# Optimization experiments

Measured on AMD Instinct MI355X. Metric: run time of the kernel, lower is better.

The kernel has to match this reference:

```python
import jax, jax.numpy as jnp
import numpy as np

B, T, F = 64, 96, 32          # batch, window_size, num_features
H_ENC, H_DEC = 128, 128       # encoder / decoder hidden sizes


def _lstm_cell(x, h, c, k, r, b):
    # Keras LSTMCell math: gates ordered i, f, g(candidate), o
    z = x @ k + h @ r + b
    i, f, g, o = jnp.split(z, 4, axis=-1)
    i = jax.nn.sigmoid(i)
    f = jax.nn.sigmoid(f)
    g = jnp.tanh(g)
    o = jax.nn.sigmoid(o)
    c_new = f * c + i * g
    h_new = o * jnp.tanh(c_new)
    return h_new, c_new


def setup_inputs() -> dict:
    key = jax.random.key(0)
    ks = jax.random.split(key, 20)
    s = 0.05
    d = {
        "inputs": jax.random.normal(ks[0], (B, T, F), jnp.float32),
        # encoder LSTMCell (input dim = F)
        "enc_k": jax.random.normal(ks[1], (F, 4 * H_ENC), jnp.float32) * s,
        "enc_r": jax.random.normal(ks[2], (H_ENC, 4 * H_ENC), jnp.float32) * s,
        "enc_b": jnp.zeros((4 * H_ENC,), jnp.float32),
        # encoder attention MLP: in = 2*H_ENC + T -> H_ENC -> 1
        "ae_w1": jax.random.normal(ks[3], (2 * H_ENC + T, H_ENC), jnp.float32) * s,
        "ae_b1": jnp.zeros((H_ENC,), jnp.float32),
        "ae_w2": jax.random.normal(ks[4], (H_ENC, 1), jnp.float32) * s,
        "ae_b2": jnp.zeros((1,), jnp.float32),
        # decoder LSTMCell (input dim = H_DEC, the fc output)
        "dec_k": jax.random.normal(ks[5], (H_DEC, 4 * H_DEC), jnp.float32) * s,
        "dec_r": jax.random.normal(ks[6], (H_DEC, 4 * H_DEC), jnp.float32) * s,
        "dec_b": jnp.zeros((4 * H_DEC,), jnp.float32),
        # decoder attention MLP: in = 2*H_DEC + H_ENC -> H_ENC -> 1
        "ad_w1": jax.random.normal(ks[7], (2 * H_DEC + H_ENC, H_ENC), jnp.float32) * s,
        "ad_b1": jnp.zeros((H_ENC,), jnp.float32),
        "ad_w2": jax.random.normal(ks[8], (H_ENC, 1), jnp.float32) * s,
        "ad_b2": jnp.zeros((1,), jnp.float32),
        # fc: (context H_ENC + y_prev 1) -> H_DEC
        "fc_w": jax.random.normal(ks[9], (H_ENC + 1, H_DEC), jnp.float32) * s,
        "fc_b": jnp.zeros((H_DEC,), jnp.float32),
        # fc_final: (d_n H_DEC + context H_ENC) -> F
        "ff_w": jax.random.normal(ks[10], (H_DEC + H_ENC, F), jnp.float32) * s,
        "ff_b": jnp.zeros((F,), jnp.float32),
    }
    return d


def reference(inputs, enc_k, enc_r, enc_b, ae_w1, ae_b1, ae_w2, ae_b2,
              dec_k, dec_r, dec_b, ad_w1, ad_b1, ad_w2, ad_b2,
              fc_w, fc_b, ff_w, ff_b):
    b, t, f = inputs.shape
    h_enc = enc_r.shape[0]
    h_dec = dec_r.shape[0]
    x_perm = jnp.transpose(inputs, (0, 2, 1))  # [B, F, T] (constant over time)

    # ---------------- encoder: input-attention LSTM over time ----------------
    def enc_step(carry, x_t):
        h, s = carry  # each [B, H_enc]
        hb = jnp.broadcast_to(h[:, None, :], (b, f, h_enc))
        sb = jnp.broadcast_to(s[:, None, :], (b, f, h_enc))
        cat = jnp.concatenate([hb, sb, x_perm], axis=2)       # [B, F, 2H+T]
        e = jnp.tanh(cat @ ae_w1 + ae_b1) @ ae_w2 + ae_b2     # [B, F, 1]
        alpha = jax.nn.softmax(e[..., 0], axis=1)             # [B, F]
        x_tilde = alpha * x_t                                 # [B, F]
        h, s = _lstm_cell(x_tilde, h, s, enc_k, enc_r, enc_b)
        return (h, s), h

    init = (jnp.zeros((b, h_enc), inputs.dtype), jnp.zeros((b, h_enc), inputs.dtype))
    _, h_all = jax.lax.scan(enc_step, init, jnp.transpose(inputs, (1, 0, 2)))
    x_encoded = jnp.transpose(h_all, (1, 0, 2))               # [B, T, H_enc]

    # ---------------- decoder: temporal-attention LSTM over time -------------
    y_prev = inputs[:, :, -1]                                 # [B, T]

    def dec_step(carry, y_t):
        d, c, _ = carry
        db = jnp.broadcast_to(d[:, None, :], (b, t, h_dec))
        cb = jnp.broadcast_to(c[:, None, :], (b, t, h_dec))
        cat = jnp.concatenate([db, cb, x_encoded], axis=2)    # [B, T, 2Hd+He]
        e = jnp.tanh(cat @ ad_w1 + ad_b1) @ ad_w2 + ad_b2     # [B, T, 1]
        beta = jax.nn.softmax(e[..., 0], axis=1)              # [B, T]
        ctx = jnp.einsum("bt,bth->bh", beta, x_encoded)       # [B, H_enc]
        y_tilde = jnp.concatenate([ctx, y_t[:, None]], axis=1) @ fc_w + fc_b
        d, c = _lstm_cell(y_tilde, d, c, dec_k, dec_r, dec_b)
        return (d, c, ctx), None

    init_d = (jnp.zeros((b, h_dec), inputs.dtype),
              jnp.zeros((b, h_dec), inputs.dtype),
              jnp.zeros((b, h_enc), inputs.dtype))
    (d_n, _, ctx), _ = jax.lax.scan(dec_step, init_d, jnp.transpose(y_prev, (1, 0)))

    y_pred = jnp.concatenate([d_n, ctx], axis=1) @ ff_w + ff_b  # [B, F]
    return y_pred[:, None, :]                                   # [B, 1, F]
```

## Files before the change

kernel.cpp:

```cpp
#include <hip/hip_runtime.h>

#define TT 96
#define FF 32
#define HH 128
#define G4 512
#define LOG2E 1.4426950408889634f

typedef _Float16 h2 __attribute__((ext_vector_type(2)));

__device__ __forceinline__ float fexp2(float x){ return __builtin_amdgcn_exp2f(x); }
__device__ __forceinline__ float frcp(float x){ return __builtin_amdgcn_rcpf(x); }
__device__ __forceinline__ float fsigmoid(float x){ return frcp(1.0f + fexp2(-LOG2E*x)); }
__device__ __forceinline__ float ftanh(float x){
    float u = fexp2(2.0f*LOG2E*x);
    return 1.0f - 2.0f*frcp(1.0f + u);
}
__device__ __forceinline__ h2 pk(float a, float b){
    h2 r; r.x = (_Float16)a; r.y = (_Float16)b; return r;
}
__device__ __forceinline__ unsigned pku(float a, float b){
    return __builtin_bit_cast(unsigned, pk(a, b));
}
__device__ __forceinline__ h2 u2h(unsigned v){ return __builtin_bit_cast(h2, v); }
__device__ __forceinline__ float fdot2(h2 a, h2 b, float c){
#if __has_builtin(__builtin_amdgcn_fdot2)
    return __builtin_amdgcn_fdot2(a, b, c, false);
#else
    return c + (float)a.x*(float)b.x + (float)a.y*(float)b.y;
#endif
}

__global__ __launch_bounds__(256) void k_prep(const float* __restrict__ fc_w,
                                              const float* __restrict__ fc_b,
                                              const float* __restrict__ dec_k,
                                              const float* __restrict__ dec_b,
                                              h2* __restrict__ Gp,
                                              float* __restrict__ gy,
                                              float* __restrict__ gb){
    int blk = blockIdx.x, tid = threadIdx.x;
    int u0 = tid, u1 = tid + 256;
    if (blk < 16){
        float a0[8], a1[8];
        #pragma unroll
        for (int r = 0; r < 8; ++r){ a0[r] = 0.f; a1[r] = 0.f; }
        for (int m = 0; m < 128; ++m){
            float d0 = dec_k[m*G4 + u0], d1 = dec_k[m*G4 + u1];
            #pragma unroll
            for (int r = 0; r < 8; ++r){
                float w = fc_w[(blk*8 + r)*HH + m];
                a0[r] += w * d0; a1[r] += w * d1;
            }
        }
        #pragma unroll
        for (int c = 0; c < 4; ++c){
            Gp[(blk*G4 + u0)*4 + c] = pk(a0[2*c], a0[2*c+1]);
            Gp[(blk*G4 + u1)*4 + c] = pk(a1[2*c], a1[2*c+1]);
        }
    } else if (blk == 16){
        float a0 = 0.f, a1 = 0.f;
        for (int m = 0; m < 128; ++m){
            float w = fc_w[128*HH + m];
            a0 += w * dec_k[m*G4 + u0]; a1 += w * dec_k[m*G4 + u1];
        }
        gy[u0] = a0; gy[u1] = a1;
    } else {
        float a0 = 0.f, a1 = 0.f;
        for (int m = 0; m < 128; ++m){
            float w = fc_b[m];
            a0 += w * dec_k[m*G4 + u0]; a1 += w * dec_k[m*G4 + u1];
        }
        gb[u0] = a0 + dec_b[u0]; gb[u1] = a1 + dec_b[u1];
    }
}

__global__ __launch_bounds__(1024, 1)
void k_enc(const float* __restrict__ inputs,
           const float* __restrict__ enc_k,
           const float* __restrict__ enc_r,
           const float* __restrict__ enc_b,
           const float* __restrict__ ae_w1,
           const float* __restrict__ ae_b1,
           const float* __restrict__ ae_w2,
           const float* __restrict__ ad_w1,
           float* __restrict__ ws_xenc,
           float* __restrict__ ws_xept){
    extern __shared__ float lds[];
    uint4* KLH4 = (uint4*)lds;
    float* XPJT = lds + 8192;
    float* XIN  = lds + 12416;
    float* HST  = lds + 15488;
    float* PP   = lds + 15744;
    float* PPZ  = lds + 16768;
    float* PE   = lds + 17792;
    float* W2E  = lds + 17920;
    float* AB1E = lds + 18048;
    h2*    HSP  = (h2*)(lds + 18176);
    h2*    XTP  = (h2*)(lds + 18240);
    uint4* WAE4 = (uint4*)(lds + 18256);
    _Float16* XEF = (_Float16*)(lds + 34640);

    const int b = blockIdx.x, tid = threadIdx.x;
    const int u = tid & 511, hf = tid >> 9;
    const int j7 = tid & 127, g8 = tid >> 7;
    const float* xin_g = inputs + b*TT*FF;

    for (int i = tid; i < TT*FF; i += 1024) XIN[i] = xin_g[i];
    for (int i = tid; i < 2048; i += 1024){
        int f8 = i >> 9, uu = i & 511;
        uint4 q;
        q.x = pku(enc_k[(f8*8+0)*G4+uu], enc_k[(f8*8+1)*G4+uu]);
        q.y = pku(enc_k[(f8*8+2)*G4+uu], enc_k[(f8*8+3)*G4+uu]);
        q.z = pku(enc_k[(f8*8+4)*G4+uu], enc_k[(f8*8+5)*G4+uu]);
        q.w = pku(enc_k[(f8*8+6)*G4+uu], enc_k[(f8*8+7)*G4+uu]);
        KLH4[i] = q;
    }
    for (int i = tid; i < 4096; i += 1024){
        int j = i & 127, i4g = i >> 7;
        int kbase = (i4g >> 2)*32 + (i4g & 3)*8;
        uint4 wv;
        wv.x = pku(ae_w1[(kbase+0)*HH + j], ae_w1[(kbase+1)*HH + j]);
        wv.y = pku(ae_w1[(kbase+2)*HH + j], ae_w1[(kbase+3)*HH + j]);
        wv.z = pku(ae_w1[(kbase+4)*HH + j], ae_w1[(kbase+5)*HH + j]);
        wv.w = pku(ae_w1[(kbase+6)*HH + j], ae_w1[(kbase+7)*HH + j]);
        WAE4[i] = wv;
    }
    if (tid < 128){ W2E[tid] = ae_w2[tid]; AB1E[tid] = ae_b1[tid]; HSP[tid] = pk(0.f, 0.f); }
    if (tid < 256) HST[tid] = 0.f;

    h2 rp_e[32];
    #pragma unroll
    for (int i = 0; i < 32; ++i)
        rp_e[i] = pk(enc_r[(hf*64 + 2*i)*G4 + u], enc_r[(hf*64 + 2*i+1)*G4 + u]);
    const float eb = (hf == 0) ? enc_b[u] : 0.f;
    __syncthreads();

    {
        int j = tid & 127, fh = tid >> 7;
        float a0=0.f, a1=0.f, a2=0.f, a3=0.f;
        for (int t = 0; t < TT; ++t){
            float w = ae_w1[(256 + t)*HH + j];
            const float* xr = &XIN[t*FF + fh*4];
            a0 += xr[0]*w; a1 += xr[1]*w; a2 += xr[2]*w; a3 += xr[3]*w;
        }
        XPJT[j*33 + fh*4 + 0] = a0;
        XPJT[j*33 + fh*4 + 1] = a1;
        XPJT[j*33 + fh*4 + 2] = a2;
        XPJT[j*33 + fh*4 + 3] = a3;
    }
    __syncthreads();

    const int f5 = tid & 31, jg5 = tid >> 5;
    float erw_e[4], iw_e[4], sumw2e = 0.f;
    #pragma unroll
    for (int i = 0; i < 4; ++i){
        float w2v = W2E[jg5*4 + i];
        float ivv = 1.0f / w2v;
        iw_e[i] = ivv;
        sumw2e += w2v;
        erw_e[i] = fexp2(2.0f*LOG2E * XPJT[(jg5*4 + i)*33 + f5]) * ivv;
    }

    const uint4* HSP4 = (const uint4*)HSP;
    const uint4* XTP4 = (const uint4*)XTP;

    for (int t = 0; t < TT; ++t){
        float z = eb;
        {
            float a0 = 0.f, a1 = 0.f;
            #pragma unroll
            for (int i4 = 0; i4 < 4; ++i4){
                uint4 q  = HSP4[g8*4 + i4];
                uint4 wv = WAE4[(g8*4 + i4)*128 + j7];
                a0 = fdot2(u2h(q.x), u2h(wv.x), a0);
                a1 = fdot2(u2h(q.y), u2h(wv.y), a1);
                a0 = fdot2(u2h(q.z), u2h(wv.z), a0);
                a1 = fdot2(u2h(q.w), u2h(wv.w), a1);
            }
            PP[tid] = a0 + a1;
        }
        if (tid < 128){
            float z2 = 0.f;
            #pragma unroll
            for (int i4 = 0; i4 < 8; ++i4){
                uint4 q = HSP4[hf*8 + i4];
                z  = fdot2(u2h(q.x), rp_e[i4*4+0], z);
                z2 = fdot2(u2h(q.y), rp_e[i4*4+1], z2);
                z  = fdot2(u2h(q.z), rp_e[i4*4+2], z);
                z2 = fdot2(u2h(q.w), rp_e[i4*4+3], z2);
            }
            z += z2;
        }
        __syncthreads();
        if (tid < 128){
            float s = AB1E[tid];
            #pragma unroll
            for (int g = 0; g < 8; ++g) s += PP[tid + 128*g];
            PE[tid] = fexp2(2.0f*LOG2E * s);
        } else {
            float z2 = 0.f;
            #pragma unroll
            for (int i4 = 0; i4 < 8; ++i4){
                uint4 q = HSP4[hf*8 + i4];
                z  = fdot2(u2h(q.x), rp_e[i4*4+0], z);
                z2 = fdot2(u2h(q.y), rp_e[i4*4+1], z2);
                z  = fdot2(u2h(q.z), rp_e[i4*4+2], z);
                z2 = fdot2(u2h(q.w), rp_e[i4*4+3], z2);
            }
            z += z2;
        }
        __syncthreads();
        {
            float acc2 = 0.f;
            #pragma unroll
            for (int i = 0; i < 4; ++i){
                float uu = PE[jg5*4 + i];
                acc2 += frcp(fmaf(erw_e[i], uu, iw_e[i]));
            }
            PP[tid] = sumw2e - 2.0f*acc2;
        }
        __syncthreads();
        if (tid < 32){
            float e = 0.f;
            #pragma unroll
            for (int g = 0; g < 32; ++g) e += PP[g*32 + tid];
            float p = fexp2(e * LOG2E);
            float ss = p;
            #pragma unroll
            for (int d = 16; d; d >>= 1) ss += __shfl_xor(ss, d, 32);
            float xt = p * frcp(ss) * XIN[t*FF + tid];
            float xt2 = __shfl_xor(xt, 1);
            if (!(tid & 1)) XTP[tid >> 1] = pk(xt, xt2);
        }
        __syncthreads();
        {
            float z2 = 0.f;
            #pragma unroll
            for (int c = 0; c < 2; ++c){
                int f8 = hf*2 + c;
                uint4 kq = KLH4[f8*512 + u];
                uint4 xq = XTP4[f8];
                z  = fdot2(u2h(kq.x), u2h(xq.x), z);
                z2 = fdot2(u2h(kq.y), u2h(xq.y), z2);
                z  = fdot2(u2h(kq.z), u2h(xq.z), z);
                z2 = fdot2(u2h(kq.w), u2h(xq.w), z2);
            }
            PPZ[hf*512 + u] = z + z2;
        }
        __syncthreads();
        if (tid < 128){
            int j = tid;
            float zi = PPZ[j]       + PPZ[512 + j];
            float zf = PPZ[128 + j] + PPZ[640 + j];
            float zg = PPZ[256 + j] + PPZ[768 + j];
            float zo = PPZ[384 + j] + PPZ[896 + j];
            float iv = fsigmoid(zi);
            float fv = fsigmoid(zf);
            float gv = ftanh(zg);
            float ov = fsigmoid(zo);
            float cn = fv * HST[128 + j] + iv * gv;
            float hn = ov * ftanh(cn);
            HST[128 + j] = cn;
            HST[j] = hn;
            ws_xenc[(b*TT + t)*HH + j] = hn;
            XEF[t*HH + j] = (_Float16)hn;
            float hn2 = __shfl_xor(hn, 1);
            float cn2 = __shfl_xor(cn, 1);
            if (!(j & 1)){
                HSP[j >> 1]        = pk(hn, hn2);
                HSP[64 + (j >> 1)] = pk(cn, cn2);
            }
        }
        __syncthreads();
    }

    {
        int j = tid & 127, th = tid >> 7;
        float acc[12];
        #pragma unroll
        for (int i = 0; i < 12; ++i) acc[i] = 0.f;
        for (int k = 0; k < 128; ++k){
            float w = ad_w1[(256 + k)*HH + j];
            #pragma unroll
            for (int i = 0; i < 12; ++i)
                acc[i] += (float)XEF[(th*12 + i)*HH + k] * w;
        }
        #pragma unroll
        for (int i = 0; i < 12; ++i)
            ws_xept[(b*HH + j)*TT + th*12 + i] = acc[i];
    }
}

__global__ __launch_bounds__(1024, 1)
void k_dec(const float* __restrict__ inputs,
           const float* __restrict__ dec_r,
           const float* __restrict__ ad_w1,
           const float* __restrict__ ad_b1,
           const float* __restrict__ ad_w2,
           const float* __restrict__ ff_w,
           const float* __restrict__ ff_b,
           const h2* __restrict__ Gp,
           const float* __restrict__ gy,
           const float* __restrict__ gb,
           const float* __restrict__ ws_xenc,
           const float* __restrict__ ws_xept,
           float* __restrict__ out){
    extern __shared__ float lds[];
    uint4* XE4 = (uint4*)lds;
    uint4* WDC4= (uint4*)(lds + 6144);
    float* PP  = lds + 22528;
    float* PPZ = lds + 23552;
    float* PPA = lds + 24576;
    float* APJ = lds + 25600;
    float* DST = lds + 25728;
    float* CTX = lds + 25984;
    float* W2L = lds + 26112;
    float* YV  = lds + 26240;
    float* SCAL= lds + 26336;
    h2*    DCP = (h2*)(lds + 26344);
    h2*    CXP = (h2*)(lds + 26408);
    h2*    BEP = (h2*)(lds + 26440);

    const int b = blockIdx.x, tid = threadIdx.x;
    const int u = tid & 511, hf = tid >> 9;
    const int j = tid & 127, og = tid >> 7;

    {
        const float* xe_g = ws_xenc + b*TT*HH;
        for (int i = tid; i < 12*HH; i += 1024){
            int t8 = i >> 7, k = i & 127;
            uint4 qq;
            qq.x = pku(xe_g[(t8*8 + 0)*HH + k], xe_g[(t8*8 + 1)*HH + k]);
            qq.y = pku(xe_g[(t8*8 + 2)*HH + k], xe_g[(t8*8 + 3)*HH + k]);
            qq.z = pku(xe_g[(t8*8 + 4)*HH + k], xe_g[(t8*8 + 5)*HH + k]);
            qq.w = pku(xe_g[(t8*8 + 6)*HH + k], xe_g[(t8*8 + 7)*HH + k]);
            XE4[i] = qq;
        }
    }
    for (int i = tid; i < 4096; i += 1024){
        int jj = i & 127, i4g = i >> 7;
        int kbase = (i4g >> 2)*32 + (i4g & 3)*8;
        uint4 wv;
        wv.x = pku(ad_w1[(kbase+0)*HH + jj], ad_w1[(kbase+1)*HH + jj]);
        wv.y = pku(ad_w1[(kbase+2)*HH + jj], ad_w1[(kbase+3)*HH + jj]);
        wv.z = pku(ad_w1[(kbase+4)*HH + jj], ad_w1[(kbase+5)*HH + jj]);
        wv.w = pku(ad_w1[(kbase+6)*HH + jj], ad_w1[(kbase+7)*HH + jj]);
        WDC4[i] = wv;
    }
    if (tid < TT) YV[tid] = inputs[b*TT*FF + tid*FF + (FF-1)];
    if (tid < 128) DCP[tid] = pk(0.f, 0.f);
    if (tid < 256) DST[tid] = 0.f;

    h2 rp[32];
    #pragma unroll
    for (int i = 0; i < 32; ++i)
        rp[i] = pk(dec_r[(hf*64 + 2*i)*G4 + u], dec_r[(hf*64 + 2*i+1)*G4 + u]);

    uint4 Greg[8];
    {
        const uint4* GQ = (const uint4*)Gp;
        #pragma unroll
        for (int g = 0; g < 8; ++g) Greg[g] = GQ[(hf*8 + g)*G4 + u];
    }

    float erw[16], iw[16], sumw2 = 0.f;
    {
        const float* xp_g = ws_xept + (b*HH + og*16)*TT + j;
        #pragma unroll
        for (int i = 0; i < 16; ++i){
            float w2v = ad_w2[og*16 + i];
            float ivv = 1.0f / w2v;
            iw[i] = ivv;
            sumw2 += w2v;
            float xp = (j < TT) ? xp_g[i*TT] : 0.f;
            erw[i] = fexp2(2.0f*LOG2E * xp) * ivv;
        }
    }

    const float gbr = gb[u], gyr = gy[u];
    const float ab1 = (tid < 128) ? ad_b1[tid] : 0.f;
    __syncthreads();

    const uint4* DCP4 = (const uint4*)DCP;
    const uint4* CXP4 = (const uint4*)CXP;
    const uint4* BEP4 = (const uint4*)BEP;

    for (int t = 0; t < TT; ++t){
        float z = (hf == 0) ? (gbr + YV[t]*gyr) : 0.f;
        {
            float s0 = 0.f, s1 = 0.f;
            #pragma unroll
            for (int i = 0; i < 4; ++i){
                uint4 dq = DCP4[og*4 + i];
                uint4 wv = WDC4[(og*4 + i)*128 + j];
                s0 = fdot2(u2h(dq.x), u2h(wv.x), s0);
                s1 = fdot2(u2h(dq.y), u2h(wv.y), s1);
                s0 = fdot2(u2h(dq.z), u2h(wv.z), s0);
                s1 = fdot2(u2h(dq.w), u2h(wv.w), s1);
            }
            PPA[og*128 + j] = s0 + s1;
        }
        if (tid < 128){
            float z2 = 0.f;
            #pragma unroll
            for (int i4 = 0; i4 < 8; ++i4){
                uint4 q = DCP4[hf*8 + i4];
                z  = fdot2(u2h(q.x), rp[i4*4+0], z);
                z2 = fdot2(u2h(q.y), rp[i4*4+1], z2);
                z  = fdot2(u2h(q.z), rp[i4*4+2], z);
                z2 = fdot2(u2h(q.w), rp[i4*4+3], z2);
            }
            z += z2;
        }
        __syncthreads();
        if (tid < 128){
            float s = ab1;
            #pragma unroll
            for (int g = 0; g < 8; ++g) s += PPA[tid + 128*g];
            APJ[tid] = fexp2(2.0f*LOG2E * s);
        } else {
            float z2 = 0.f;
            #pragma unroll
            for (int i4 = 0; i4 < 8; ++i4){
                uint4 q = DCP4[hf*8 + i4];
                z  = fdot2(u2h(q.x), rp[i4*4+0], z);
                z2 = fdot2(u2h(q.y), rp[i4*4+1], z2);
                z  = fdot2(u2h(q.z), rp[i4*4+2], z);
                z2 = fdot2(u2h(q.w), rp[i4*4+3], z2);
            }
            z += z2;
        }
        __syncthreads();
        {
            float acc = 0.f;
            if (j < TT){
                float acc2 = 0.f;
                #pragma unroll
                for (int q4 = 0; q4 < 4; ++q4){
                    float4 uj = *(const float4*)&APJ[og*16 + q4*4];
                    acc2 += frcp(fmaf(erw[q4*4+0], uj.x, iw[q4*4+0]));
                    acc2 += frcp(fmaf(erw[q4*4+1], uj.y, iw[q4*4+1]));
                    acc2 += frcp(fmaf(erw[q4*4+2], uj.z, iw[q4*4+2]));
                    acc2 += frcp(fmaf(erw[q4*4+3], uj.w, iw[q4*4+3]));
                }
                acc = sumw2 - 2.0f*acc2;
            }
            PP[tid] = acc;
        }
        __syncthreads();
        if (tid < 64){
            float ea = 0.f;
            #pragma unroll
            for (int g = 0; g < 8; ++g) ea += PP[tid + 128*g];
            float pa = fexp2(ea * LOG2E);
            float pb = 0.f;
            if (tid < 32){
                float ebv = 0.f;
                #pragma unroll
                for (int g = 0; g < 8; ++g) ebv += PP[64 + tid + 128*g];
                pb = fexp2(ebv * LOG2E);
            }
            float ss = pa + pb;
            #pragma unroll
            for (int d = 32; d; d >>= 1) ss += __shfl_xor(ss, d, 64);
            float pa2 = __shfl_xor(pa, 1);
            float pb2 = __shfl_xor(pb, 1);
            if (!(tid & 1)){
                BEP[tid >> 1] = pk(pa, pa2);
                if (tid < 32) BEP[32 + (tid >> 1)] = pk(pb, pb2);
            }
            if (tid == 0) SCAL[0] = frcp(ss);
        }
        __syncthreads();
        if (tid < 128){
            float s0 = 0.f, s1 = 0.f;
            #pragma unroll
            for (int t8 = 0; t8 < 12; t8 += 2){
                uint4 xq0 = XE4[t8*HH + tid],     bb0 = BEP4[t8];
                uint4 xq1 = XE4[(t8+1)*HH + tid], bb1 = BEP4[t8+1];
                s0 = fdot2(u2h(xq0.x), u2h(bb0.x), s0);
                s1 = fdot2(u2h(xq0.y), u2h(bb0.y), s1);
                s0 = fdot2(u2h(xq0.z), u2h(bb0.z), s0);
                s1 = fdot2(u2h(xq0.w), u2h(bb0.w), s1);
                s0 = fdot2(u2h(xq1.x), u2h(bb1.x), s0);
                s1 = fdot2(u2h(xq1.y), u2h(bb1.y), s1);
                s0 = fdot2(u2h(xq1.z), u2h(bb1.z), s0);
                s1 = fdot2(u2h(xq1.w), u2h(bb1.w), s1);
            }
            float cv = (s0 + s1) * SCAL[0];
            CTX[tid] = cv;
            float cv2 = __shfl_xor(cv, 1);
            if (!(tid & 1)) CXP[tid >> 1] = pk(cv, cv2);
        }
        __syncthreads();
        {
            float z2 = 0.f;
            #pragma unroll
            for (int gi = 0; gi < 8; ++gi){
                uint4 q  = Greg[gi];
                uint4 cc = CXP4[hf*8 + gi];
                z  = fdot2(u2h(q.x), u2h(cc.x), z);
                z2 = fdot2(u2h(q.y), u2h(cc.y), z2);
                z  = fdot2(u2h(q.z), u2h(cc.z), z);
                z2 = fdot2(u2h(q.w), u2h(cc.w), z2);
            }
            PPZ[hf*512 + u] = z + z2;
        }
        __syncthreads();
        if (tid < 128){
            int jj = tid;
            float zi = PPZ[jj]       + PPZ[512 + jj];
            float zf = PPZ[128 + jj] + PPZ[640 + jj];
            float zg = PPZ[256 + jj] + PPZ[768 + jj];
            float zo = PPZ[384 + jj] + PPZ[896 + jj];
            float iv = fsigmoid(zi);
            float fv = fsigmoid(zf);
            float gv = ftanh(zg);
            float ov = fsigmoid(zo);
            float cn = fv * DST[128 + jj] + iv * gv;
            float hn = ov * ftanh(cn);
            DST[128 + jj] = cn;
            DST[jj] = hn;
            float hn2 = __shfl_xor(hn, 1);
            float cn2 = __shfl_xor(cn, 1);
            if (!(jj & 1)){
                DCP[jj >> 1]        = pk(hn, hn2);
                DCP[64 + (jj >> 1)] = pk(cn, cn2);
            }
        }
        __syncthreads();
    }

    {
        int jp = tid & 31, sg = tid >> 5;
        float a = 0.f;
        #pragma unroll
        for (int kk = 0; kk < 8; ++kk){
            int k = sg*8 + kk;
            float val = (k < 128) ? DST[k] : CTX[k - 128];
            a += val * ff_w[k*FF + jp];
        }
        PP[sg*32 + jp] = a;
    }
    __syncthreads();
    if (tid < 32){
        float o = ff_b[tid];
        #pragma unroll
        for (int s = 0; s < 32; ++s) o += PP[s*32 + tid];
        out[b*FF + tid] = o;
    }
}

extern "C" void kernel_launch(void* const* d_in, const int* in_sizes, int n_in,
                              void* d_out, int out_size, void* d_ws, size_t ws_size,
                              hipStream_t stream) {
    const float* inputs = (const float*)d_in[0];
    const float* enc_k  = (const float*)d_in[1];
    const float* enc_r  = (const float*)d_in[2];
    const float* enc_b  = (const float*)d_in[3];
    const float* ae_w1  = (const float*)d_in[4];
    const float* ae_b1  = (const float*)d_in[5];
    const float* ae_w2  = (const float*)d_in[6];
    const float* dec_k  = (const float*)d_in[8];
    const float* dec_r  = (const float*)d_in[9];
    const float* dec_b  = (const float*)d_in[10];
    const float* ad_w1  = (const float*)d_in[11];
    const float* ad_b1  = (const float*)d_in[12];
    const float* ad_w2  = (const float*)d_in[13];
    const float* fc_w   = (const float*)d_in[15];
    const float* fc_b   = (const float*)d_in[16];
    const float* ff_w   = (const float*)d_in[17];
    const float* ff_b   = (const float*)d_in[18];

    float* ws      = (float*)d_ws;
    float* ws_xenc = ws;
    float* ws_xept = ws + 786432;
    h2*    Gp      = (h2*)(ws + 1572864);
    float* gy      = ws + 1605632;
    float* gb      = ws + 1606144;

    hipFuncSetAttribute((const void*)k_enc, hipFuncAttributeMaxDynamicSharedMemorySize, 163136);
    hipFuncSetAttribute((const void*)k_dec, hipFuncAttributeMaxDynamicSharedMemorySize, 105888);

    k_prep<<<18, 256, 0, stream>>>(fc_w, fc_b, dec_k, dec_b, Gp, gy, gb);
    k_enc<<<64, 1024, 163136, stream>>>(inputs, enc_k, enc_r, enc_b, ae_w1, ae_b1, ae_w2,
                                        ad_w1, ws_xenc, ws_xept);
    k_dec<<<64, 1024, 105888, stream>>>(inputs, dec_r, ad_w1, ad_b1, ad_w2, ff_w, ff_b,
                                        Gp, gy, gb, ws_xenc, ws_xept, (float*)d_out);
}
```

Measured before the change: 697.1 us.

## Fold prep kernel into encoder launch and keep attention weights in registers

Merges the k_prep weight-folding work into extra blocks of the encoder launch, removing one kernel launch and its serialization. The encoder's per-thread slice of ae_w1 now lives in registers instead of LDS, which shrinks dynamic shared memory and removes per-step LDS loads. The attention-energy algebra is restated to multiply by w2 outside the reciprocal, and the 32-way column reduction is split across 64 threads with a shuffle. The trade-offs are higher register pressure and some extra LDS reads of W2E on every timestep.

Result: faster. 660.6 us (-5.2%).

```diff
diff --git a/kernel.cpp b/kernel.cpp
--- a/kernel.cpp
+++ b/kernel.cpp
@@ -28,49 +28,6 @@
 #else
     return c + (float)a.x*(float)b.x + (float)a.y*(float)b.y;
 #endif
-}
-
-__global__ __launch_bounds__(256) void k_prep(const float* __restrict__ fc_w,
-                                              const float* __restrict__ fc_b,
-                                              const float* __restrict__ dec_k,
-                                              const float* __restrict__ dec_b,
-                                              h2* __restrict__ Gp,
-                                              float* __restrict__ gy,
-                                              float* __restrict__ gb){
-    int blk = blockIdx.x, tid = threadIdx.x;
-    int u0 = tid, u1 = tid + 256;
-    if (blk < 16){
-        float a0[8], a1[8];
-        #pragma unroll
-        for (int r = 0; r < 8; ++r){ a0[r] = 0.f; a1[r] = 0.f; }
-        for (int m = 0; m < 128; ++m){
-            float d0 = dec_k[m*G4 + u0], d1 = dec_k[m*G4 + u1];
-            #pragma unroll
-            for (int r = 0; r < 8; ++r){
-                float w = fc_w[(blk*8 + r)*HH + m];
-                a0[r] += w * d0; a1[r] += w * d1;
-            }
-        }
-        #pragma unroll
-        for (int c = 0; c < 4; ++c){
-            Gp[(blk*G4 + u0)*4 + c] = pk(a0[2*c], a0[2*c+1]);
-            Gp[(blk*G4 + u1)*4 + c] = pk(a1[2*c], a1[2*c+1]);
-        }
-    } else if (blk == 16){
-        float a0 = 0.f, a1 = 0.f;
-        for (int m = 0; m < 128; ++m){
-            float w = fc_w[128*HH + m];
-            a0 += w * dec_k[m*G4 + u0]; a1 += w * dec_k[m*G4 + u1];
-        }
-        gy[u0] = a0; gy[u1] = a1;
-    } else {
-        float a0 = 0.f, a1 = 0.f;
-        for (int m = 0; m < 128; ++m){
-            float w = fc_b[m];
-            a0 += w * dec_k[m*G4 + u0]; a1 += w * dec_k[m*G4 + u1];
-        }
-        gb[u0] = a0 + dec_b[u0]; gb[u1] = a1 + dec_b[u1];
-    }
 }
 
 __global__ __launch_bounds__(1024, 1)
@@ -82,8 +39,54 @@
            const float* __restrict__ ae_b1,
            const float* __restrict__ ae_w2,
            const float* __restrict__ ad_w1,
+           const float* __restrict__ fc_w,
+           const float* __restrict__ fc_b,
+           const float* __restrict__ dec_k,
+           const float* __restrict__ dec_b,
+           h2* __restrict__ Gp,
+           float* __restrict__ gy,
+           float* __restrict__ gb,
            float* __restrict__ ws_xenc,
            float* __restrict__ ws_xept){
+    if (blockIdx.x >= 64){
+        int blk = blockIdx.x - 64, tid = threadIdx.x;
+        if (tid >= 256) return;
+        int u0 = tid, u1 = tid + 256;
+        if (blk < 16){
+            float a0[8], a1[8];
+            #pragma unroll
+            for (int r = 0; r < 8; ++r){ a0[r] = 0.f; a1[r] = 0.f; }
+            for (int m = 0; m < 128; ++m){
+                float d0 = dec_k[m*G4 + u0], d1 = dec_k[m*G4 + u1];
+                #pragma unroll
+                for (int r = 0; r < 8; ++r){
+                    float w = fc_w[(blk*8 + r)*HH + m];
+                    a0[r] += w * d0; a1[r] += w * d1;
+                }
+            }
+            #pragma unroll
+            for (int c = 0; c < 4; ++c){
+                Gp[(blk*G4 + u0)*4 + c] = pk(a0[2*c], a0[2*c+1]);
+                Gp[(blk*G4 + u1)*4 + c] = pk(a1[2*c], a1[2*c+1]);
+            }
+        } else if (blk == 16){
+            float a0 = 0.f, a1 = 0.f;
+            for (int m = 0; m < 128; ++m){
+                float w = fc_w[128*HH + m];
+                a0 += w * dec_k[m*G4 + u0]; a1 += w * dec_k[m*G4 + u1];
+            }
+            gy[u0] = a0; gy[u1] = a1;
+        } else {
+            float a0 = 0.f, a1 = 0.f;
+            for (int m = 0; m < 128; ++m){
+                float w = fc_b[m];
+                a0 += w * dec_k[m*G4 + u0]; a1 += w * dec_k[m*G4 + u1];
+            }
+            gb[u0] = a0 + dec_b[u0]; gb[u1] = a1 + dec_b[u1];
+        }
+        return;
+    }
+
     extern __shared__ float lds[];
     uint4* KLH4 = (uint4*)lds;
     float* XPJT = lds + 8192;
@@ -96,8 +99,7 @@
     float* AB1E = lds + 18048;
     h2*    HSP  = (h2*)(lds + 18176);
     h2*    XTP  = (h2*)(lds + 18240);
-    uint4* WAE4 = (uint4*)(lds + 18256);
-    _Float16* XEF = (_Float16*)(lds + 34640);
+    _Float16* XEF = (_Float16*)(lds + 18248);
 
     const int b = blockIdx.x, tid = threadIdx.x;
     const int u = tid & 511, hf = tid >> 9;
@@ -114,16 +116,6 @@
         q.w = pku(enc_k[(f8*8+6)*G4+uu], enc_k[(f8*8+7)*G4+uu]);
         KLH4[i] = q;
     }
-    for (int i = tid; i < 4096; i += 1024){
-        int j = i & 127, i4g = i >> 7;
-        int kbase = (i4g >> 2)*32 + (i4g & 3)*8;
-        uint4 wv;
-        wv.x = pku(ae_w1[(kbase+0)*HH + j], ae_w1[(kbase+1)*HH + j]);
-        wv.y = pku(ae_w1[(kbase+2)*HH + j], ae_w1[(kbase+3)*HH + j]);
-        wv.z = pku(ae_w1[(kbase+4)*HH + j], ae_w1[(kbase+5)*HH + j]);
-        wv.w = pku(ae_w1[(kbase+6)*HH + j], ae_w1[(kbase+7)*HH + j]);
-        WAE4[i] = wv;
-    }
     if (tid < 128){ W2E[tid] = ae_w2[tid]; AB1E[tid] = ae_b1[tid]; HSP[tid] = pk(0.f, 0.f); }
     if (tid < 256) HST[tid] = 0.f;
 
@@ -131,6 +123,17 @@
     #pragma unroll
     for (int i = 0; i < 32; ++i)
         rp_e[i] = pk(enc_r[(hf*64 + 2*i)*G4 + u], enc_r[(hf*64 + 2*i+1)*G4 + u]);
+
+    uint4 wae[4];
+    #pragma unroll
+    for (int i4 = 0; i4 < 4; ++i4){
+        int r0 = (g8*4 + i4)*8;
+        wae[i4].x = pku(ae_w1[(r0+0)*HH + j7], ae_w1[(r0+1)*HH + j7]);
+        wae[i4].y = pku(ae_w1[(r0+2)*HH + j7], ae_w1[(r0+3)*HH + j7]);
+        wae[i4].z = pku(ae_w1[(r0+4)*HH + j7], ae_w1[(r0+5)*HH + j7]);
+        wae[i4].w = pku(ae_w1[(r0+6)*HH + j7], ae_w1[(r0+7)*HH + j7]);
+    }
+
     const float eb = (hf == 0) ? enc_b[u] : 0.f;
     __syncthreads();
 
@@ -150,14 +153,11 @@
     __syncthreads();
 
     const int f5 = tid & 31, jg5 = tid >> 5;
-    float erw_e[4], iw_e[4], sumw2e = 0.f;
+    float er_e[4], sumw2e = 0.f;
     #pragma unroll
     for (int i = 0; i < 4; ++i){
-        float w2v = W2E[jg5*4 + i];
-        float ivv = 1.0f / w2v;
-        iw_e[i] = ivv;
-        sumw2e += w2v;
-        erw_e[i] = fexp2(2.0f*LOG2E * XPJT[(jg5*4 + i)*33 + f5]) * ivv;
+        er_e[i] = fexp2(2.0f*LOG2E * XPJT[(jg5*4 + i)*33 + f5]);
+        sumw2e += W2E[jg5*4 + i];
     }
 
     const uint4* HSP4 = (const uint4*)HSP;
@@ -170,7 +170,7 @@
             #pragma unroll
             for (int i4 = 0; i4 < 4; ++i4){
                 uint4 q  = HSP4[g8*4 + i4];
-                uint4 wv = WAE4[(g8*4 + i4)*128 + j7];
+                uint4 wv = wae[i4];
                 a0 = fdot2(u2h(q.x), u2h(wv.x), a0);
                 a1 = fdot2(u2h(q.y), u2h(wv.y), a1);
                 a0 = fdot2(u2h(q.z), u2h(wv.z), a0);
@@ -214,22 +214,27 @@
             #pragma unroll
             for (int i = 0; i < 4; ++i){
                 float uu = PE[jg5*4 + i];
-                acc2 += frcp(fmaf(erw_e[i], uu, iw_e[i]));
+                float w  = W2E[jg5*4 + i];
+                acc2 += w * frcp(fmaf(er_e[i], uu, 1.0f));
             }
             PP[tid] = sumw2e - 2.0f*acc2;
         }
         __syncthreads();
-        if (tid < 32){
+        if (tid < 64){
+            int f = tid & 31, hh = tid >> 5;
             float e = 0.f;
             #pragma unroll
-            for (int g = 0; g < 32; ++g) e += PP[g*32 + tid];
+            for (int g = 0; g < 16; ++g) e += PP[(hh*16 + g)*32 + f];
+            e += __shfl_xor(e, 32, 64);
             float p = fexp2(e * LOG2E);
             float ss = p;
             #pragma unroll
             for (int d = 16; d; d >>= 1) ss += __shfl_xor(ss, d, 32);
-            float xt = p * frcp(ss) * XIN[t*FF + tid];
-            float xt2 = __shfl_xor(xt, 1);
-            if (!(tid & 1)) XTP[tid >> 1] = pk(xt, xt2);
+            if (tid < 32){
+                float xt = p * frcp(ss) * XIN[t*FF + tid];
+                float xt2 = __shfl_xor(xt, 1);
+                if (!(tid & 1)) XTP[tid >> 1] = pk(xt, xt2);
+            }
         }
         __syncthreads();
         {
@@ -578,12 +583,12 @@
     float* gy      = ws + 1605632;
     float* gb      = ws + 1606144;
 
-    hipFuncSetAttribute((const void*)k_enc, hipFuncAttributeMaxDynamicSharedMemorySize, 163136);
+    hipFuncSetAttribute((const void*)k_enc, hipFuncAttributeMaxDynamicSharedMemorySize, 97568);
     hipFuncSetAttribute((const void*)k_dec, hipFuncAttributeMaxDynamicSharedMemorySize, 105888);
 
-    k_prep<<<18, 256, 0, stream>>>(fc_w, fc_b, dec_k, dec_b, Gp, gy, gb);
-    k_enc<<<64, 1024, 163136, stream>>>(inputs, enc_k, enc_r, enc_b, ae_w1, ae_b1, ae_w2,
-                                        ad_w1, ws_xenc, ws_xept);
+    k_enc<<<82, 1024, 97568, stream>>>(inputs, enc_k, enc_r, enc_b, ae_w1, ae_b1, ae_w2,
+                                       ad_w1, fc_w, fc_b, dec_k, dec_b, Gp, gy, gb,
+                                       ws_xenc, ws_xept);
     k_dec<<<64, 1024, 105888, stream>>>(inputs, dec_r, ad_w1, ad_b1, ad_w2, ff_w, ff_b,
                                         Gp, gy, gb, ws_xenc, ws_xept, (float*)d_out);
 }
```
